# Performance work log

Measured on AMD Instinct MI355X. Metric: run time of the kernel, lower is better.

## Reference

```python
import jax, jax.numpy as jnp
import numpy as np

EPS_BN = 1e-5      # torch BatchNorm2d default eps
EPS_NORM = 1e-12   # torch F.normalize default eps
NEG_FILL = -1e18


def _bn(h, gamma, beta, mean, var):
    # eval-mode BatchNorm2d over channel axis 1 of NCHW
    scale = (gamma / jnp.sqrt(var + EPS_BN))[None, :, None, None]
    return h * scale + (beta - mean * gamma / jnp.sqrt(var + EPS_BN))[None, :, None, None]


def _l2norm(v, axis):
    n = jnp.linalg.norm(v, axis=axis, keepdims=True)
    return v / jnp.maximum(n, EPS_NORM)


def setup_inputs() -> dict:
    key = jax.random.key(0)
    ks = jax.random.split(key, 6)
    bs, num, dim, K = 16, 8192, 128, 64
    return {
        "x_": jax.random.normal(ks[0], (bs, num, dim), jnp.float32),
        "conv1_w": jax.random.normal(ks[1], (dim, 1, 3, 3), jnp.float32) * 0.1,
        "bn1_gamma": jnp.ones((dim,), jnp.float32),
        "bn1_beta": jnp.zeros((dim,), jnp.float32),
        "bn1_mean": jnp.zeros((dim,), jnp.float32),
        "bn1_var": jnp.ones((dim,), jnp.float32),
        "conv2_w": jax.random.normal(ks[2], (K, dim, 1, 1), jnp.float32) * 0.05,
        "conv2_b": jax.random.normal(ks[3], (K,), jnp.float32) * 0.05,
        "bn2_gamma": jnp.ones((K,), jnp.float32),
        "bn2_beta": jnp.zeros((K,), jnp.float32),
        "bn2_mean": jnp.zeros((K,), jnp.float32),
        "bn2_var": jnp.ones((K,), jnp.float32),
        "centroids": 0.1 * jax.random.uniform(ks[4], (K, dim), jnp.float32),
        "length": jax.random.randint(ks[5], (bs,), 1, num + 1).astype(jnp.int32),
    }


def reference(x_, conv1_w, bn1_gamma, bn1_beta, bn1_mean, bn1_var,
              conv2_w, conv2_b, bn2_gamma, bn2_beta, bn2_mean, bn2_var,
              centroids, length):
    N, T, C = x_.shape
    K = centroids.shape[0]
    # [N, T, C] -> [N, C, T, 1] (input_modal='textual'/'region' branch)
    x = jnp.transpose(x_, (0, 2, 1))[..., None]
    # descriptor-wise L2 norm over channels (normalize_input=True)
    x = _l2norm(x, axis=1)
    # depthwise 3x3 conv, padding 1, no bias
    h = jax.lax.conv_general_dilated(
        x, conv1_w, window_strides=(1, 1), padding=((1, 1), (1, 1)),
        dimension_numbers=("NCHW", "OIHW", "NCHW"), feature_group_count=C)
    h = jax.nn.relu(_bn(h, bn1_gamma, bn1_beta, bn1_mean, bn1_var))
    # pointwise 1x1 conv (as matmul) + bias
    h = jnp.einsum("ncto,kc->nkto", h, conv2_w[:, :, 0, 0]) + conv2_b[None, :, None, None]
    h = jax.nn.relu(_bn(h, bn2_gamma, bn2_beta, bn2_mean, bn2_var))
    soft_assign = h.reshape(N, K, T)
    # textual path: mask padded positions before softmax over clusters
    valid = jnp.arange(T)[None, :] < length[:, None]          # [N, T]
    soft_assign = jnp.where(valid[:, None, :], soft_assign, NEG_FILL)
    a = jax.nn.softmax(soft_assign, axis=1)                   # [N, K, T]
    x_flat = x[..., 0]                                        # [N, C, T]
    # fused VLAD: sum_t a[n,k,t]*(x[n,c,t] - centroid[k,c]) as two matmuls
    vlad = jnp.einsum("nkt,nct->nkc", a, x_flat) - a.sum(-1)[:, :, None] * centroids[None]
    vlad = _l2norm(vlad, axis=2)           # intra-normalization
    vlad = vlad.reshape(N, K * x_flat.shape[1])
    vlad = _l2norm(vlad, axis=1)           # global L2 norm
    return vlad
```

## Files before the change

kernel.cpp:

```cpp
#include <hip/hip_runtime.h>
#include <math.h>

#define N_ 16
#define T_ 8192
#define C_ 128
#define K_ 64

#define TPB_A 128
#define BPN_A 64
#define TCH 256
#define NCH 32

#define NW_ASUM 0
#define NW_GSUM 1024
#define NW_MCS  2048
#define NW_W2F  4096
#define NW_P1   8192
#define NW_XTM  8960
#define NW_AG   8397568
#define NW_PART 12591872
#define NW_TOTAL 16786176

typedef __attribute__((ext_vector_type(8))) short short8;
typedef __attribute__((ext_vector_type(4))) float f32x4;

__device__ __forceinline__ uint bfr(float f) {
    uint u = __float_as_uint(f);
    return (u + 0x7fffu + ((u >> 16) & 1u)) >> 16;
}
__device__ __forceinline__ uint pack2(float lo, float hi) {
    return bfr(lo) | (bfr(hi) << 16);
}
__device__ __forceinline__ float bfu(ushort u) {
    return __uint_as_float(((uint)u) << 16);
}

__global__ void setup_k(const float* __restrict__ conv1_w,
                        const float* __restrict__ bn1_g, const float* __restrict__ bn1_b,
                        const float* __restrict__ bn1_m, const float* __restrict__ bn1_v,
                        const float* __restrict__ conv2_w,
                        const float* __restrict__ bn2_g, const float* __restrict__ bn2_v,
                        ushort* __restrict__ w2t, float* __restrict__ p1,
                        float* __restrict__ zr, int zcnt) {
    const int gt = blockIdx.x * 256 + threadIdx.x;
    for (int idx = gt; idx < 8192; idx += 1024) {
        int j = idx & 7;
        int lane = (idx >> 3) & 63;
        int mq = idx >> 9;
        int m = mq >> 2, q = mq & 3;
        int fr = lane & 15, fg = lane >> 4;
        int k = m * 16 + fr;
        float sck = bn2_g[k] * rsqrtf(bn2_v[k] + 1e-5f);
        float v = conv2_w[k * C_ + q * 32 + fg * 8 + j] * sck;
        w2t[idx] = (ushort)bfr(v);
    }
    for (int c = gt; c < C_; c += 1024) {
        float s1 = bn1_g[c] * rsqrtf(bn1_v[c] + 1e-5f);
        p1[c]       = conv1_w[c * 9 + 1] * s1;
        p1[128 + c] = conv1_w[c * 9 + 4] * s1;
        p1[256 + c] = conv1_w[c * 9 + 7] * s1;
        p1[384 + c] = bn1_b[c] - bn1_m[c] * s1;
    }
    for (int i = gt; i < zcnt; i += 1024) zr[i] = 0.0f;
}

__global__ __launch_bounds__(256, 8) void xnorm_k(const float* __restrict__ x,
                                                  ushort* __restrict__ xtm,
                                                  const int* __restrict__ length,
                                                  float* __restrict__ mcs) {
    __shared__ uint xt[32][64];
    const int tid = threadIdx.x;
    const int lane = tid & 63;
    const int w = tid >> 6;
    const int n = blockIdx.x >> 8;
    const int tloc = (blockIdx.x & 255) * 32;
    const size_t row0 = (size_t)blockIdx.x * 32;
    const int L = length[n];
    const int Lc = ((L + 255) >> 8) << 8;

#pragma unroll
    for (int i = 0; i < 8; ++i) {
        int r = w * 8 + i;
        const float* xr = x + (row0 + r) * C_;
        float2 v = *(const float2*)&xr[lane * 2];
        float ss = v.x * v.x + v.y * v.y;
#pragma unroll
        for (int m = 1; m < 64; m <<= 1) ss += __shfl_xor(ss, m, 64);
        float rn = 1.0f / fmaxf(sqrtf(ss), 1e-12f);
        xt[r][lane] = pack2(v.x * rn, v.y * rn);
    }
    __syncthreads();

    if (tloc <= Lc) {
        uint4* dst = (uint4*)(xtm + (size_t)blockIdx.x * 4096);
#pragma unroll
        for (int uu = 0; uu < 2; ++uu) {
            int u = tid * 2 + uu;
            int c = u >> 2, j = u & 3;
            int cw = c >> 1, sh = (c & 1) * 16;
            uint o[4];
#pragma unroll
            for (int q = 0; q < 4; ++q) {
                uint lo = (xt[j * 8 + q * 2][cw] >> sh) & 0xffffu;
                uint hi = (xt[j * 8 + q * 2 + 1][cw] >> sh) & 0xffffu;
                o[q] = lo | (hi << 16);
            }
            uint4 v; v.x = o[0]; v.y = o[1]; v.z = o[2]; v.w = o[3];
            dst[u] = v;
        }
    }
    if (tloc >= Lc && w == 0) {
        float sx = 0.f, sy = 0.f;
#pragma unroll 8
        for (int r = 0; r < 32; ++r) {
            uint u = xt[r][lane];
            sx += bfu((ushort)(u & 0xffffu));
            sy += bfu((ushort)(u >> 16));
        }
        atomicAdd(&mcs[n * C_ + lane * 2], sx);
        atomicAdd(&mcs[n * C_ + lane * 2 + 1], sy);
    }
}

__global__ __launch_bounds__(256, 3) void assign2_k(
    const ushort* __restrict__ xtm,
    const float* __restrict__ conv2_b,
    const float* __restrict__ bn2_g, const float* __restrict__ bn2_b,
    const float* __restrict__ bn2_m, const float* __restrict__ bn2_v,
    const int* __restrict__ length,
    const ushort* __restrict__ w2t, const float* __restrict__ p1,
    ushort* __restrict__ agall) {

    __shared__ __align__(16) ushort w2l[8192];
    __shared__ __align__(16) ushort h_s[4][16 * 136];
    __shared__ __align__(16) uint4 ab[2][64 * 5];

    const int tid = threadIdx.x;
    const int lane = tid & 63;
    const int w = tid >> 6;
    const int fr = lane & 15, fg = lane >> 4;
    const int tile = w >> 1, half = w & 1;
    const int n = blockIdx.x >> 6;
    const int tb = (blockIdx.x & (BPN_A - 1)) * TPB_A;
    const int L = length[n];
    if (tb >= L) return;

    const ushort* xtm_n = xtm + (size_t)n * 256 * 4096;

    {
        const uint4* w2g = (const uint4*)w2t;
        uint4* w2d = (uint4*)w2l;
#pragma unroll
        for (int i = 0; i < 4; ++i) w2d[tid + i * 256] = w2g[tid + i * 256];
    }

    float wa[2], wbv[2], wcv[2], sbv[2];
#pragma unroll
    for (int p = 0; p < 2; ++p) {
        int c = lane + p * 64;
        wa[p] = p1[c]; wbv[p] = p1[128 + c];
        wcv[p] = p1[256 + c]; sbv[p] = p1[384 + c];
    }

    float sh2r[16];
#pragma unroll
    for (int m = 0; m < 4; ++m)
#pragma unroll
        for (int r = 0; r < 4; ++r) {
            int k = m * 16 + fg * 4 + r;
            float s = bn2_g[k] * rsqrtf(bn2_v[k] + 1e-5f);
            sh2r[m * 4 + r] = s * conv2_b[k] + bn2_b[k] - bn2_m[k] * s;
        }

    ushort* ag = agall + (size_t)n * (T_ / 32) * 2048;
    __syncthreads();

    for (int s = 0; s < TPB_A / 64; ++s) {
        const int tbs = tb + s * 64;
        if (tbs >= L) continue;
        const int tcs = (tbs >> 5) + tile;
        const ushort* xch = xtm_n + (size_t)tcs * 4096;
        const int t0 = tbs + tile * 32 + half * 16;

        if (t0 < L) {
            ushort* hw = h_s[w];
#pragma unroll
            for (int p = 0; p < 2; ++p) {
                const int c = lane + p * 64;
                short8 x0 = *(const short8*)&xch[c * 32 + half * 16];
                short8 x1 = *(const short8*)&xch[c * 32 + half * 16 + 8];
                float av[18];
                av[0] = 0.f; av[17] = 0.f;
                if (t0 > 0)
                    av[0] = bfu(half ? xch[c * 32 + 15] : xch[c * 32 - 4096 + 31]);
                if (t0 + 16 < T_)
                    av[17] = bfu(half ? xch[c * 32 + 4096] : xch[c * 32 + 16]);
#pragma unroll
                for (int j = 0; j < 8; ++j) {
                    av[1 + j] = bfu((ushort)x0[j]);
                    av[9 + j] = bfu((ushort)x1[j]);
                }
                float WA = wa[p], WB = wbv[p], WC = wcv[p], SB = sbv[p];
#pragma unroll
                for (int j = 0; j < 16; ++j)
                    hw[j * 136 + c] = (ushort)bfr(
                        fmaxf(0.f, av[j] * WA + av[j + 1] * WB + av[j + 2] * WC + SB));
            }
            f32x4 accL[4];
#pragma unroll
            for (int m = 0; m < 4; ++m) accL[m] = (f32x4){0.f, 0.f, 0.f, 0.f};
            const ushort* hbp = h_s[w] + fr * 136 + fg * 8;
#pragma unroll
            for (int q = 0; q < 4; ++q) {
                short8 hf = *(const short8*)(hbp + q * 32);
                short8 w0 = *(const short8*)&w2l[((0 * 4 + q) * 64 + lane) * 8];
                short8 w1 = *(const short8*)&w2l[((1 * 4 + q) * 64 + lane) * 8];
                short8 w2f = *(const short8*)&w2l[((2 * 4 + q) * 64 + lane) * 8];
                short8 w3 = *(const short8*)&w2l[((3 * 4 + q) * 64 + lane) * 8];
                accL[0] = __builtin_amdgcn_mfma_f32_16x16x32_bf16(w0, hf, accL[0], 0, 0, 0);
                accL[1] = __builtin_amdgcn_mfma_f32_16x16x32_bf16(w1, hf, accL[1], 0, 0, 0);
                accL[2] = __builtin_amdgcn_mfma_f32_16x16x32_bf16(w2f, hf, accL[2], 0, 0, 0);
                accL[3] = __builtin_amdgcn_mfma_f32_16x16x32_bf16(w3, hf, accL[3], 0, 0, 0);
            }
            {
                int t = t0 + fr;
                float v[16];
#pragma unroll
                for (int m = 0; m < 4; ++m)
#pragma unroll
                    for (int r = 0; r < 4; ++r)
                        v[m * 4 + r] = fmaxf(0.f, accL[m][r] + sh2r[m * 4 + r]);
                if (t < L) {
                    float mx = v[0];
#pragma unroll
                    for (int i = 1; i < 16; ++i) mx = fmaxf(mx, v[i]);
                    mx = fmaxf(mx, __shfl_xor(mx, 16, 64));
                    mx = fmaxf(mx, __shfl_xor(mx, 32, 64));
                    float se = 0.f;
#pragma unroll
                    for (int i = 0; i < 16; ++i) { v[i] = __expf(v[i] - mx); se += v[i]; }
                    se += __shfl_xor(se, 16, 64);
                    se += __shfl_xor(se, 32, 64);
                    float inv = 1.0f / se;
#pragma unroll
                    for (int i = 0; i < 16; ++i) v[i] *= inv;
                } else {
#pragma unroll
                    for (int i = 0; i < 16; ++i) v[i] = 0.015625f;
                }
                const int jq = half * 2 + (fr >> 3);
                const int te = fr & 7;
#pragma unroll
                for (int m = 0; m < 4; ++m)
#pragma unroll
                    for (int r = 0; r < 4; ++r) {
                        int k = m * 16 + fg * 4 + r;
                        ((ushort*)&ab[tile][k * 5 + jq])[te] = (ushort)bfr(v[m * 4 + r]);
                    }
            }
        } else {
            uint4 ones;
            ones.x = ones.y = ones.z = ones.w = 0x3C803C80u;
            ab[tile][lane * 5 + half * 2] = ones;
            ab[tile][lane * 5 + half * 2 + 1] = ones;
        }
        __syncthreads();
#pragma unroll
        for (int tt = 0; tt < 2; ++tt) {
            uint4 v = ab[tt][(tid >> 2) * 5 + (tid & 3)];
            *((uint4*)(ag + (size_t)(tbs / 32 + tt) * 2048) + tid) = v;
        }
        __syncthreads();
    }
}

__global__ __launch_bounds__(256, 4) void vlad2_k(
    const ushort* __restrict__ xtm, const ushort* __restrict__ agall,
    const int* __restrict__ length, float* __restrict__ part,
    float* __restrict__ asum) {

    const int tid = threadIdx.x;
    const int lane = tid & 63;
    const int w = tid >> 6;
    const int fr = lane & 15, fg = lane >> 4;
    const int n = blockIdx.x >> 5;
    const int chunk = blockIdx.x & (NCH - 1);
    const int tb = chunk * TCH;
    const int L = length[n];
    if (tb >= L) return;

    const ushort* xn_n = xtm + (size_t)n * 256 * 4096;
    const ushort* ag = agall + (size_t)n * (T_ / 32) * 2048;

    short8 onesf;
    {
        short f = (fr == 0) ? (short)0x3F80 : (short)0;
#pragma unroll
        for (int j = 0; j < 8; ++j) onesf[j] = f;
    }

    f32x4 accB[9];
#pragma unroll
    for (int cb = 0; cb < 9; ++cb) accB[cb] = (f32x4){0.f, 0.f, 0.f, 0.f};

#pragma unroll
    for (int st = 0; st < TCH / 32; ++st) {
        const int t0 = tb + st * 32;
        const int tc = t0 >> 5;
        short8 af;
        if (t0 < L) {
            af = *(const short8*)(ag + (size_t)tc * 2048 + (w * 16 + fr) * 32 + fg * 8);
        } else {
#pragma unroll
            for (int j = 0; j < 8; ++j) af[j] = (short)0x3C80;
        }
        const ushort* xch = xn_n + (size_t)tc * 4096;
#pragma unroll
        for (int cb = 0; cb < 8; ++cb) {
            short8 bfv = *(const short8*)&xch[(cb * 16 + fr) * 32 + fg * 8];
            accB[cb] = __builtin_amdgcn_mfma_f32_16x16x32_bf16(af, bfv, accB[cb], 0, 0, 0);
        }
        accB[8] = __builtin_amdgcn_mfma_f32_16x16x32_bf16(af, onesf, accB[8], 0, 0, 0);
    }

    float* pr = part + (size_t)(n * NCH + chunk) * (K_ * C_);
#pragma unroll
    for (int cb = 0; cb < 8; ++cb)
#pragma unroll
        for (int r = 0; r < 4; ++r)
            pr[(w * 16 + fg * 4 + r) * C_ + cb * 16 + fr] = accB[cb][r];
    if (fr == 0) {
#pragma unroll
        for (int r = 0; r < 4; ++r)
            atomicAdd(&asum[n * K_ + w * 16 + fg * 4 + r], accB[8][r]);
    }
}

__global__ void finalize2_k(const float* __restrict__ cent,
                            const float* __restrict__ part,
                            const float* __restrict__ asum,
                            const float* __restrict__ mcs,
                            const int* __restrict__ length,
                            float* __restrict__ gsum, float* __restrict__ out) {
    int row = blockIdx.x * 4 + (threadIdx.x >> 6);
    int lane = threadIdx.x & 63;
    int n = row >> 6, k = row & 63;
    const int L = length[n];
    const int nlive = (L + 255) >> 8;
    const float* pr = part + (size_t)n * NCH * (K_ * C_) + k * C_;
    float y0 = 0.f, y1 = 0.f;
#pragma unroll 4
    for (int b = 0; b < nlive; ++b) {
        y0 += pr[(size_t)b * (K_ * C_) + lane];
        y1 += pr[(size_t)b * (K_ * C_) + lane + 64];
    }
    y0 += 0.015625f * mcs[n * C_ + lane];
    y1 += 0.015625f * mcs[n * C_ + lane + 64];
    float as = asum[row] + (float)(T_ - nlive * 256) * 0.015625f;
    y0 -= as * cent[k * C_ + lane];
    y1 -= as * cent[k * C_ + lane + 64];
    float ss = y0 * y0 + y1 * y1;
#pragma unroll
    for (int m = 1; m < 64; m <<= 1) ss += __shfl_xor(ss, m, 64);
    float rs = 1.0f / fmaxf(sqrtf(ss), 1e-12f);
    out[(size_t)row * C_ + lane] = y0 * rs;
    out[(size_t)row * C_ + lane + 64] = y1 * rs;
    if (lane == 0) atomicAdd(&gsum[n], ss * rs * rs);
}

__global__ void gscale2_k(float* __restrict__ out, const float* __restrict__ gsum) {
    int idx = blockIdx.x * 256 + threadIdx.x;
    int n = idx >> 13;
    out[idx] *= 1.0f / fmaxf(sqrtf(gsum[n]), 1e-12f);
}

extern "C" void kernel_launch(void* const* d_in, const int* in_sizes, int n_in,
                              void* d_out, int out_size, void* d_ws, size_t ws_size,
                              hipStream_t stream) {
    const float* x       = (const float*)d_in[0];
    const float* conv1_w = (const float*)d_in[1];
    const float* bn1_g   = (const float*)d_in[2];
    const float* bn1_b   = (const float*)d_in[3];
    const float* bn1_m   = (const float*)d_in[4];
    const float* bn1_v   = (const float*)d_in[5];
    const float* conv2_w = (const float*)d_in[6];
    const float* conv2_b = (const float*)d_in[7];
    const float* bn2_g   = (const float*)d_in[8];
    const float* bn2_b   = (const float*)d_in[9];
    const float* bn2_m   = (const float*)d_in[10];
    const float* bn2_v   = (const float*)d_in[11];
    const float* cent    = (const float*)d_in[12];
    const int*   length  = (const int*)d_in[13];
    float* out = (float*)d_out;
    float* ws  = (float*)d_ws;

    setup_k<<<4, 256, 0, stream>>>(conv1_w, bn1_g, bn1_b, bn1_m, bn1_v,
                                   conv2_w, bn2_g, bn2_v,
                                   (ushort*)(ws + NW_W2F), ws + NW_P1,
                                   ws, 4096);
    xnorm_k<<<N_ * T_ / 32, 256, 0, stream>>>(x, (ushort*)(ws + NW_XTM),
                                              length, ws + NW_MCS);
    assign2_k<<<N_ * BPN_A, 256, 0, stream>>>(
        (const ushort*)(ws + NW_XTM), conv2_b, bn2_g, bn2_b, bn2_m, bn2_v,
        length, (const ushort*)(ws + NW_W2F), ws + NW_P1,
        (ushort*)(ws + NW_AG));
    vlad2_k<<<N_ * NCH, 256, 0, stream>>>(
        (const ushort*)(ws + NW_XTM), (const ushort*)(ws + NW_AG),
        length, ws + NW_PART, ws + NW_ASUM);
    finalize2_k<<<(N_ * K_) / 4, 256, 0, stream>>>(
        cent, ws + NW_PART, ws + NW_ASUM, ws + NW_MCS, length,
        ws + NW_GSUM, out);
    gscale2_k<<<(N_ * K_ * C_) / 256, 256, 0, stream>>>(out, ws + NW_GSUM);
}
```

Measured before the change: 87.31 us.

## Fuse soft-assignment and VLAD accumulation kernels, dropping the assignment buffer

Merges the assignment kernel and the VLAD matmul kernel into one. Each block now feeds its soft-assignment tile straight from LDS into MFMA accumulation against the normalized x chunks, instead of writing the assignments to global memory and reading them back in a second launch. Partial sums are now kept per 128-token block instead of per 256-token chunk. That doubles the partial buffer that finalize must reduce, and the heavier fused kernel may lose occupancy at launch_bounds(256,3).

```diff
diff --git a/kernel.cpp b/kernel.cpp
--- a/kernel.cpp
+++ b/kernel.cpp
@@ -8,8 +8,6 @@
 
 #define TPB_A 128
 #define BPN_A 64
-#define TCH 256
-#define NCH 32
 
 #define NW_ASUM 0
 #define NW_GSUM 1024
@@ -17,8 +15,7 @@
 #define NW_W2F  4096
 #define NW_P1   8192
 #define NW_XTM  8960
-#define NW_AG   8397568
-#define NW_PART 12591872
+#define NW_PART 8397568
 #define NW_TOTAL 16786176
 
 typedef __attribute__((ext_vector_type(8))) short short8;
@@ -76,7 +73,7 @@
     const int tloc = (blockIdx.x & 255) * 32;
     const size_t row0 = (size_t)blockIdx.x * 32;
     const int L = length[n];
-    const int Lc = ((L + 255) >> 8) << 8;
+    const int Lb = ((L + 127) >> 7) << 7;
 
 #pragma unroll
     for (int i = 0; i < 8; ++i) {
@@ -91,7 +88,7 @@
     }
     __syncthreads();
 
-    if (tloc <= Lc) {
+    if (tloc <= Lb) {
         uint4* dst = (uint4*)(xtm + (size_t)blockIdx.x * 4096);
 #pragma unroll
         for (int uu = 0; uu < 2; ++uu) {
@@ -109,7 +106,7 @@
             dst[u] = v;
         }
     }
-    if (tloc >= Lc && w == 0) {
+    if (tloc >= Lb && w == 0) {
         float sx = 0.f, sy = 0.f;
 #pragma unroll 8
         for (int r = 0; r < 32; ++r) {
@@ -122,14 +119,14 @@
     }
 }
 
-__global__ __launch_bounds__(256, 3) void assign2_k(
+__global__ __launch_bounds__(256, 3) void fused_k(
     const ushort* __restrict__ xtm,
     const float* __restrict__ conv2_b,
     const float* __restrict__ bn2_g, const float* __restrict__ bn2_b,
     const float* __restrict__ bn2_m, const float* __restrict__ bn2_v,
     const int* __restrict__ length,
     const ushort* __restrict__ w2t, const float* __restrict__ p1,
-    ushort* __restrict__ agall) {
+    float* __restrict__ part, float* __restrict__ asum) {
 
     __shared__ __align__(16) ushort w2l[8192];
     __shared__ __align__(16) ushort h_s[4][16 * 136];
@@ -141,7 +138,8 @@
     const int fr = lane & 15, fg = lane >> 4;
     const int tile = w >> 1, half = w & 1;
     const int n = blockIdx.x >> 6;
-    const int tb = (blockIdx.x & (BPN_A - 1)) * TPB_A;
+    const int blk = blockIdx.x & (BPN_A - 1);
+    const int tb = blk * TPB_A;
     const int L = length[n];
     if (tb >= L) return;
 
@@ -172,12 +170,21 @@
             sh2r[m * 4 + r] = s * conv2_b[k] + bn2_b[k] - bn2_m[k] * s;
         }
 
-    ushort* ag = agall + (size_t)n * (T_ / 32) * 2048;
+    short8 onesf;
+    {
+        short f = (fr == 0) ? (short)0x3F80 : (short)0;
+#pragma unroll
+        for (int j = 0; j < 8; ++j) onesf[j] = f;
+    }
+
+    f32x4 accB[9];
+#pragma unroll
+    for (int cb = 0; cb < 9; ++cb) accB[cb] = (f32x4){0.f, 0.f, 0.f, 0.f};
+
     __syncthreads();
 
     for (int s = 0; s < TPB_A / 64; ++s) {
         const int tbs = tb + s * 64;
-        if (tbs >= L) continue;
         const int tcs = (tbs >> 5) + tile;
         const ushort* xch = xtm_n + (size_t)tcs * 4096;
         const int t0 = tbs + tile * 32 + half * 16;
@@ -259,71 +266,27 @@
                     }
             }
         } else {
-            uint4 ones;
-            ones.x = ones.y = ones.z = ones.w = 0x3C803C80u;
-            ab[tile][lane * 5 + half * 2] = ones;
-            ab[tile][lane * 5 + half * 2 + 1] = ones;
+            uint4 cfill;
+            cfill.x = cfill.y = cfill.z = cfill.w = 0x3C803C80u;
+            ab[tile][lane * 5 + half * 2] = cfill;
+            ab[tile][lane * 5 + half * 2 + 1] = cfill;
         }
         __syncthreads();
 #pragma unroll
-        for (int tt = 0; tt < 2; ++tt) {
-            uint4 v = ab[tt][(tid >> 2) * 5 + (tid & 3)];
-            *((uint4*)(ag + (size_t)(tbs / 32 + tt) * 2048) + tid) = v;
+        for (int cc = 0; cc < 2; ++cc) {
+            const ushort* xc2 = xtm_n + (size_t)((tbs >> 5) + cc) * 4096;
+            short8 af = *(const short8*)&ab[cc][(w * 16 + fr) * 5 + fg];
+#pragma unroll
+            for (int cb = 0; cb < 8; ++cb) {
+                short8 bfv = *(const short8*)&xc2[(cb * 16 + fr) * 32 + fg * 8];
+                accB[cb] = __builtin_amdgcn_mfma_f32_16x16x32_bf16(af, bfv, accB[cb], 0, 0, 0);
+            }
+            accB[8] = __builtin_amdgcn_mfma_f32_16x16x32_bf16(af, onesf, accB[8], 0, 0, 0);
         }
         __syncthreads();
     }
-}
-
-__global__ __launch_bounds__(256, 4) void vlad2_k(
-    const ushort* __restrict__ xtm, const ushort* __restrict__ agall,
-    const int* __restrict__ length, float* __restrict__ part,
-    float* __restrict__ asum) {
-
-    const int tid = threadIdx.x;
-    const int lane = tid & 63;
-    const int w = tid >> 6;
-    const int fr = lane & 15, fg = lane >> 4;
-    const int n = blockIdx.x >> 5;
-    const int chunk = blockIdx.x & (NCH - 1);
-    const int tb = chunk * TCH;
-    const int L = length[n];
-    if (tb >= L) return;
-
-    const ushort* xn_n = xtm + (size_t)n * 256 * 4096;
-    const ushort* ag = agall + (size_t)n * (T_ / 32) * 2048;
-
-    short8 onesf;
-    {
-        short f = (fr == 0) ? (short)0x3F80 : (short)0;
-#pragma unroll
-        for (int j = 0; j < 8; ++j) onesf[j] = f;
-    }
-
-    f32x4 accB[9];
-#pragma unroll
-    for (int cb = 0; cb < 9; ++cb) accB[cb] = (f32x4){0.f, 0.f, 0.f, 0.f};
-
-#pragma unroll
-    for (int st = 0; st < TCH / 32; ++st) {
-        const int t0 = tb + st * 32;
-        const int tc = t0 >> 5;
-        short8 af;
-        if (t0 < L) {
-            af = *(const short8*)(ag + (size_t)tc * 2048 + (w * 16 + fr) * 32 + fg * 8);
-        } else {
-#pragma unroll
-            for (int j = 0; j < 8; ++j) af[j] = (short)0x3C80;
-        }
-        const ushort* xch = xn_n + (size_t)tc * 4096;
-#pragma unroll
-        for (int cb = 0; cb < 8; ++cb) {
-            short8 bfv = *(const short8*)&xch[(cb * 16 + fr) * 32 + fg * 8];
-            accB[cb] = __builtin_amdgcn_mfma_f32_16x16x32_bf16(af, bfv, accB[cb], 0, 0, 0);
-        }
-        accB[8] = __builtin_amdgcn_mfma_f32_16x16x32_bf16(af, onesf, accB[8], 0, 0, 0);
-    }
-
-    float* pr = part + (size_t)(n * NCH + chunk) * (K_ * C_);
+
+    float* pr = part + (size_t)(n * BPN_A + blk) * (K_ * C_);
 #pragma unroll
     for (int cb = 0; cb < 8; ++cb)
 #pragma unroll
@@ -346,8 +309,8 @@
     int lane = threadIdx.x & 63;
     int n = row >> 6, k = row & 63;
     const int L = length[n];
-    const int nlive = (L + 255) >> 8;
-    const float* pr = part + (size_t)n * NCH * (K_ * C_) + k * C_;
+    const int nlive = (L + 127) >> 7;
+    const float* pr = part + (size_t)n * BPN_A * (K_ * C_) + k * C_;
     float y0 = 0.f, y1 = 0.f;
 #pragma unroll 4
     for (int b = 0; b < nlive; ++b) {
@@ -356,7 +319,7 @@
     }
     y0 += 0.015625f * mcs[n * C_ + lane];
     y1 += 0.015625f * mcs[n * C_ + lane + 64];
-    float as = asum[row] + (float)(T_ - nlive * 256) * 0.015625f;
+    float as = asum[row] + (float)(T_ - nlive * 128) * 0.015625f;
     y0 -= as * cent[k * C_ + lane];
     y1 -= as * cent[k * C_ + lane + 64];
     float ss = y0 * y0 + y1 * y1;
@@ -400,13 +363,10 @@
                                    ws, 4096);
     xnorm_k<<<N_ * T_ / 32, 256, 0, stream>>>(x, (ushort*)(ws + NW_XTM),
                                               length, ws + NW_MCS);
-    assign2_k<<<N_ * BPN_A, 256, 0, stream>>>(
+    fused_k<<<N_ * BPN_A, 256, 0, stream>>>(
         (const ushort*)(ws + NW_XTM), conv2_b, bn2_g, bn2_b, bn2_m, bn2_v,
         length, (const ushort*)(ws + NW_W2F), ws + NW_P1,
-        (ushort*)(ws + NW_AG));
-    vlad2_k<<<N_ * NCH, 256, 0, stream>>>(
-        (const ushort*)(ws + NW_XTM), (const ushort*)(ws + NW_AG),
-        length, ws + NW_PART, ws + NW_ASUM);
+        ws + NW_PART, ws + NW_ASUM);
     finalize2_k<<<(N_ * K_) / 4, 256, 0, stream>>>(
         cent, ws + NW_PART, ws + NW_ASUM, ws + NW_MCS, length,
         ws + NW_GSUM, out);
```

Result: faster. 80.85 us (-7.4%).
